# Kernel optimization log

Hardware: AMD Instinct MI355X
Metric: run time of the kernel (lower is better)

## Reference

```python
import jax, jax.numpy as jnp
import numpy as np

N, T, FS, FD, GH, RH, E = 100000, 24, 32, 8, 32, 64, 3200000


def spmm(edge_row, edge_col, edge_val, X):
    # out[i] = sum_e val[e] * X[col[e]]  for edges with row[e]==i
    return jax.ops.segment_sum(edge_val[:, None] * X[edge_col], edge_row, num_segments=N)


def setup_inputs() -> dict:
    key = jax.random.key(0)
    ks = jax.random.split(key, 20)
    s = 0.05
    return {
        "X_static": jax.random.normal(ks[0], (N, FS), jnp.float32),
        "X_dyn_mean": jax.random.normal(ks[1], (T, N, FD), jnp.float32),
        "edge_row": jax.random.randint(ks[2], (E,), 0, N, jnp.int32),
        "edge_col": jax.random.randint(ks[3], (E,), 0, N, jnp.int32),
        "edge_val": jax.random.uniform(ks[4], (E,), jnp.float32),
        # GraphConv layers
        "g1_W": jax.random.normal(ks[5], (GH, FS), jnp.float32) * s,
        "g1_b": jnp.zeros((GH,), jnp.float32),
        "g2_W": jax.random.normal(ks[6], (GH, GH), jnp.float32) * s,
        "g2_b": jnp.zeros((GH,), jnp.float32),
        # GRU (PyTorch layout: 3H rows = [r, z, n])
        "W_ih": jax.random.normal(ks[7], (3 * RH, GH + FD), jnp.float32) * s,
        "W_hh": jax.random.normal(ks[8], (3 * RH, RH), jnp.float32) * s,
        "b_ih": jnp.zeros((3 * RH,), jnp.float32),
        "b_hh": jnp.zeros((3 * RH,), jnp.float32),
        # MLP head
        "h1_W": jax.random.normal(ks[9], (64, RH), jnp.float32) * s,
        "h1_b": jnp.zeros((64,), jnp.float32),
        "h2_W": jax.random.normal(ks[10], (1, 64), jnp.float32) * s,
        "h2_b": jnp.zeros((1,), jnp.float32),
    }


def reference(X_static, X_dyn_mean, edge_row, edge_col, edge_val,
              g1_W, g1_b, g2_W, g2_b, W_ih, W_hh, b_ih, b_hh,
              h1_W, h1_b, h2_W, h2_b):
    # GraphConv x2: linear then sparse A_hat @ Xw, ReLU
    h = jax.nn.relu(spmm(edge_row, edge_col, edge_val, X_static @ g1_W.T + g1_b))
    h = jax.nn.relu(spmm(edge_row, edge_col, edge_val, h @ g2_W.T + g2_b))  # (N, GH)

    # z_t = concat([h, X_dyn_mean[t]], -1); precompute input-gate projections
    z_seq = jnp.concatenate([jnp.broadcast_to(h[None], (T, N, GH)), X_dyn_mean], axis=-1)  # (T,N,GH+FD)
    gi_all = jnp.einsum('tnd,hd->tnh', z_seq, W_ih) + b_ih  # (T,N,3H)

    def step(hs, gi):
        gh = hs @ W_hh.T + b_hh
        i_r, i_z, i_n = jnp.split(gi, 3, axis=-1)
        h_r, h_z, h_n = jnp.split(gh, 3, axis=-1)
        r = jax.nn.sigmoid(i_r + h_r)
        zg = jax.nn.sigmoid(i_z + h_z)
        n = jnp.tanh(i_n + r * h_n)
        h_new = (1.0 - zg) * n + zg * hs
        return h_new, h_new

    h0 = jnp.zeros((N, RH), jnp.float32)
    _, out = jax.lax.scan(step, h0, gi_all)  # (T,N,RH)

    y = jax.nn.relu(out @ h1_W.T + h1_b)
    y = jax.nn.sigmoid(y @ h2_W.T + h2_b)[..., 0]  # (T,N)
    return y
```

## Files before the change

### kernel.cpp

```cpp
#include <hip/hip_runtime.h>
#include <math.h>

typedef short bf16x8_t __attribute__((ext_vector_type(8)));
typedef float f32x4_t  __attribute__((ext_vector_type(4)));

__device__ __forceinline__ float fast_rcp(float x) { return __builtin_amdgcn_rcpf(x); }
__device__ __forceinline__ float sigmoidf_(float x) {
  return fast_rcp(1.0f + __expf(-x));
}
__device__ __forceinline__ float tanhf_(float x) {
  return fmaf(-2.0f, fast_rcp(__expf(2.0f * x) + 1.0f), 1.0f);
}
__device__ __forceinline__ unsigned short f2bf(float f) {
  unsigned int u = __float_as_uint(f);
  unsigned int r = (u + 0x7fffu + ((u >> 16) & 1u)) >> 16;
  return (unsigned short)r;
}
__device__ __forceinline__ float bf2f(unsigned short u) {
  return __uint_as_float(((unsigned int)u) << 16);
}
__device__ __forceinline__ unsigned int cvt_pk_bf16(float a, float b) {
  unsigned int d;
  asm("v_cvt_pk_bf16_f32 %0, %1, %2" : "=v"(d) : "v"(a), "v"(b));
  return d;
}

template<bool RELU_IN, bool OUT_BF16>
__global__ __launch_bounds__(256) void lin32_kernel(
    const float* __restrict__ X, const float* __restrict__ W,
    const float* __restrict__ b, void* __restrict__ outp, int N)
{
  __shared__ float sW[32][33];
  __shared__ float sb[32];
  __shared__ float sX[8][33];
  const int tid = threadIdx.x;
  for (int i = tid; i < 1024; i += 256) sW[i >> 5][i & 31] = W[i];
  if (tid < 32) sb[tid] = b[tid];
  const int n0 = blockIdx.x * 8;
  {
    float v = X[(size_t)n0 * 32 + tid];
    if (RELU_IN) v = fmaxf(v, 0.0f);
    sX[tid >> 5][tid & 31] = v;
  }
  __syncthreads();
  const int ln = tid >> 5, f = tid & 31;
  float acc = sb[f];
  #pragma unroll
  for (int j = 0; j < 32; j++) acc += sX[ln][j] * sW[f][j];
  if (OUT_BF16) ((unsigned short*)outp)[(size_t)n0 * 32 + tid] = f2bf(acc);
  else          ((float*)outp)[(size_t)n0 * 32 + tid] = acc;
}

__global__ __launch_bounds__(256) void spmm_kernel(
    const int* __restrict__ erow, const int* __restrict__ ecol,
    const float* __restrict__ eval, const float* __restrict__ X,
    float* __restrict__ out, int E)
{
  const long gid = (long)blockIdx.x * 256 + threadIdx.x;
  const int e = (int)(gid >> 3);
  const int q = (int)(gid & 7);
  if (e >= E) return;
  const int r = erow[e], c = ecol[e];
  const float v = eval[e];
  const float4 x = *(const float4*)(X + (size_t)c * 32 + q * 4);
  float* o = out + (size_t)r * 32 + q * 4;
  atomicAdd(o + 0, v * x.x);
  atomicAdd(o + 1, v * x.y);
  atomicAdd(o + 2, v * x.z);
  atomicAdd(o + 3, v * x.w);
}

#define BROWS 128
#define BSHIFT 7
#define EPB 8192
#define MAXBUCKETS 1024

__global__ __launch_bounds__(256) void hist_bin_k(
    const int* __restrict__ erow, int* __restrict__ blockHist,
    int E, int nBuckets)
{
  __shared__ int h[MAXBUCKETS];
  for (int i = threadIdx.x; i < nBuckets; i += 256) h[i] = 0;
  __syncthreads();
  const int e0 = blockIdx.x * EPB;
  const int cnt = min(E - e0, EPB);
  for (int i = threadIdx.x; i < cnt; i += 256)
    atomicAdd(&h[erow[e0 + i] >> BSHIFT], 1);
  __syncthreads();
  int* o = blockHist + (size_t)blockIdx.x * nBuckets;
  for (int i = threadIdx.x; i < nBuckets; i += 256) o[i] = h[i];
}

__global__ __launch_bounds__(128) void colscan_k(
    int* __restrict__ blockHist, int* __restrict__ bucketTotal,
    int nb, int nBuckets)
{
  __shared__ int s[128];
  const int b = blockIdx.x;
  const int t = threadIdx.x;
  const int k = (nb + 127) >> 7;
  const int i0 = t * k, i1 = min(nb, i0 + k);
  int p = 0;
  for (int i = i0; i < i1; i++) p += blockHist[(size_t)i * nBuckets + b];
  s[t] = p;
  __syncthreads();
  #pragma unroll
  for (int off = 1; off < 128; off <<= 1) {
    int u = (t >= off) ? s[t - off] : 0;
    __syncthreads(); s[t] += u; __syncthreads();
  }
  int run = s[t] - p;
  if (t == 127) bucketTotal[b] = s[127];
  for (int i = i0; i < i1; i++) {
    int* q = &blockHist[(size_t)i * nBuckets + b];
    int v = *q;
    *q = run;
    run += v;
  }
}

__global__ __launch_bounds__(1024) void bucketstart_k(
    const int* __restrict__ bucketTotal, int* __restrict__ bucketStart,
    int nBuckets)
{
  __shared__ int s[1024];
  const int b = threadIdx.x;
  int v = (b < nBuckets) ? bucketTotal[b] : 0;
  s[b] = v;
  __syncthreads();
  for (int off = 1; off < 1024; off <<= 1) {
    int u = (b >= off) ? s[b - off] : 0;
    __syncthreads(); s[b] += u; __syncthreads();
  }
  if (b < nBuckets) bucketStart[b] = s[b] - v;
  if (b == nBuckets - 1) bucketStart[nBuckets] = s[b];
}

__global__ __launch_bounds__(256) void scatter_stage_k(
    const int* __restrict__ erow, const int* __restrict__ ecol,
    const float* __restrict__ evl, const int* __restrict__ blockOfs,
    const int* __restrict__ bucketStart, int2* __restrict__ binned,
    int E, int nBuckets)
{
  __shared__ int2 rec[EPB];
  __shared__ int  dstv[EPB];
  __shared__ int  cur[MAXBUCKETS];
  __shared__ int  gb[MAXBUCKETS];
  __shared__ int  part[256];
  const int tid = threadIdx.x;
  const int e0 = blockIdx.x * EPB;
  const int cntE = min(E - e0, EPB);
  const int* ofs = blockOfs + (size_t)blockIdx.x * nBuckets;

  for (int i = tid; i < nBuckets; i += 256) cur[i] = 0;
  __syncthreads();
  for (int i = tid; i < cntE; i += 256)
    atomicAdd(&cur[erow[e0 + i] >> BSHIFT], 1);
  __syncthreads();

  const int k = (nBuckets + 255) >> 8;
  const int i0 = tid * k, i1 = min(i0 + k, nBuckets);
  int s = 0;
  for (int i = i0; i < i1; i++) s += cur[i];
  part[tid] = s;
  __syncthreads();
  for (int off = 1; off < 256; off <<= 1) {
    int u = (tid >= off) ? part[tid - off] : 0;
    __syncthreads(); part[tid] += u; __syncthreads();
  }
  int run = part[tid] - s;
  for (int i = i0; i < i1; i++) {
    int hv = cur[i];
    gb[i] = bucketStart[i] + ofs[i] - run;
    cur[i] = run;
    run += hv;
  }
  __syncthreads();

  for (int i = tid; i < cntE; i += 256) {
    int r = erow[e0 + i];
    int c = ecol[e0 + i];
    float v = evl[e0 + i];
    int b = r >> BSHIFT;
    int p = atomicAdd(&cur[b], 1);
    rec[p]  = make_int2(((r & (BROWS - 1)) << 17) | c, __float_as_int(v));
    dstv[p] = gb[b];
  }
  __syncthreads();

  for (int i = tid; i < cntE; i += 256)
    binned[dstv[i] + i] = rec[i];
}

__global__ __launch_bounds__(512) void bucket_sort_k(
    const int* __restrict__ bucketStart, const int2* __restrict__ binned,
    int2* __restrict__ pairs, int* __restrict__ startv, int* __restrict__ cnt,
    int N)
{
  __shared__ int h[BROWS], sc[BROWS], cur[BROWS];
  const int tid = threadIdx.x;
  const int bkt = blockIdx.x;
  const int s = bucketStart[bkt], e = bucketStart[bkt + 1];
  if (tid < BROWS) h[tid] = 0;
  __syncthreads();
  for (int i = s + tid; i < e; i += 512)
    atomicAdd(&h[((unsigned)binned[i].x) >> 17], 1);
  __syncthreads();
  if (tid < BROWS) sc[tid] = h[tid];
  __syncthreads();
  #pragma unroll
  for (int off = 1; off < BROWS; off <<= 1) {
    int u = (tid < BROWS && tid >= off) ? sc[tid - off] : 0;
    __syncthreads();
    if (tid < BROWS) sc[tid] += u;
    __syncthreads();
  }
  if (tid < BROWS) {
    int start = s + sc[tid] - h[tid];
    cur[tid] = start;
    int row = (bkt << BSHIFT) + tid;
    if (row < N) { startv[row] = start; cnt[row] = h[tid]; }
  }
  __syncthreads();
  for (int i = s + tid; i < e; i += 512) {
    int2 r = binned[i];
    int p = atomicAdd(&cur[((unsigned)r.x) >> 17], 1);
    pairs[p] = make_int2(r.x & 0x1ffff, r.y);
  }
}

__global__ __launch_bounds__(256) void hist_k(const int* __restrict__ erow, int* cnt, int E) {
  int e = blockIdx.x * 256 + threadIdx.x;
  if (e < E) atomicAdd(&cnt[erow[e]], 1);
}

__global__ __launch_bounds__(256) void scan1_k(const int* __restrict__ cnt, int* startv, int* bsum, int N) {
  __shared__ int s[256];
  int t = threadIdx.x, i = blockIdx.x * 256 + t;
  int v = (i < N) ? cnt[i] : 0;
  s[t] = v; __syncthreads();
  for (int off = 1; off < 256; off <<= 1) {
    int u = (t >= off) ? s[t - off] : 0;
    __syncthreads(); s[t] += u; __syncthreads();
  }
  if (i < N) startv[i] = s[t] - v;
  if (t == 255) bsum[blockIdx.x] = s[255];
}

__global__ __launch_bounds__(512) void scan2_k(const int* __restrict__ bsum, int* bsumx, int nb) {
  __shared__ int s[512];
  int t = threadIdx.x;
  int v = (t < nb) ? bsum[t] : 0;
  s[t] = v; __syncthreads();
  for (int off = 1; off < 512; off <<= 1) {
    int u = (t >= off) ? s[t - off] : 0;
    __syncthreads(); s[t] += u; __syncthreads();
  }
  if (t < nb) bsumx[t] = s[t] - v;
}

__global__ __launch_bounds__(256) void scan3_k(int* startv, const int* __restrict__ bsumx, int* cursor, int N) {
  int i = blockIdx.x * 256 + threadIdx.x;
  if (i < N) {
    int v = startv[i] + bsumx[i >> 8];
    startv[i] = v;
    cursor[i] = v;
  }
}

__global__ __launch_bounds__(256) void scatter_k(
    const int* __restrict__ erow, const int* __restrict__ ecol,
    const float* __restrict__ evl, int* cursor, int2* __restrict__ pairs, int E)
{
  int e = blockIdx.x * 256 + threadIdx.x;
  if (e < E) {
    int r = erow[e];
    int p = atomicAdd(&cursor[r], 1);
    pairs[p] = make_int2(ecol[e], __float_as_int(evl[e]));
  }
}

__global__ __launch_bounds__(256) void spmm_csr_bf16_k(
    const int* __restrict__ startv, const int* __restrict__ cnt,
    const int2* __restrict__ pairs, const unsigned short* __restrict__ X,
    float* __restrict__ out, int N)
{
  int row = blockIdx.x * 4 + (threadIdx.x >> 6);
  if (row >= N) return;
  int lane = threadIdx.x & 63;
  int f = lane & 31, hh = lane >> 5;
  int start = startv[row];
  int len = cnt[row];
  int half = len >> 1;
  int base = start + (hh ? half : 0);
  int n = hh ? (len - half) : half;
  float acc = 0.0f;
  int i = 0;
  for (; i + 7 < n; i += 8) {
    int2 p0 = pairs[base + i + 0];
    int2 p1 = pairs[base + i + 1];
    int2 p2 = pairs[base + i + 2];
    int2 p3 = pairs[base + i + 3];
    int2 p4 = pairs[base + i + 4];
    int2 p5 = pairs[base + i + 5];
    int2 p6 = pairs[base + i + 6];
    int2 p7 = pairs[base + i + 7];
    float x0 = bf2f(X[(size_t)p0.x * 32 + f]);
    float x1 = bf2f(X[(size_t)p1.x * 32 + f]);
    float x2 = bf2f(X[(size_t)p2.x * 32 + f]);
    float x3 = bf2f(X[(size_t)p3.x * 32 + f]);
    float x4 = bf2f(X[(size_t)p4.x * 32 + f]);
    float x5 = bf2f(X[(size_t)p5.x * 32 + f]);
    float x6 = bf2f(X[(size_t)p6.x * 32 + f]);
    float x7 = bf2f(X[(size_t)p7.x * 32 + f]);
    acc = fmaf(__int_as_float(p0.y), x0, acc);
    acc = fmaf(__int_as_float(p1.y), x1, acc);
    acc = fmaf(__int_as_float(p2.y), x2, acc);
    acc = fmaf(__int_as_float(p3.y), x3, acc);
    acc = fmaf(__int_as_float(p4.y), x4, acc);
    acc = fmaf(__int_as_float(p5.y), x5, acc);
    acc = fmaf(__int_as_float(p6.y), x6, acc);
    acc = fmaf(__int_as_float(p7.y), x7, acc);
  }
  for (; i + 3 < n; i += 4) {
    int2 p0 = pairs[base + i + 0];
    int2 p1 = pairs[base + i + 1];
    int2 p2 = pairs[base + i + 2];
    int2 p3 = pairs[base + i + 3];
    float x0 = bf2f(X[(size_t)p0.x * 32 + f]);
    float x1 = bf2f(X[(size_t)p1.x * 32 + f]);
    float x2 = bf2f(X[(size_t)p2.x * 32 + f]);
    float x3 = bf2f(X[(size_t)p3.x * 32 + f]);
    acc = fmaf(__int_as_float(p0.y), x0, acc);
    acc = fmaf(__int_as_float(p1.y), x1, acc);
    acc = fmaf(__int_as_float(p2.y), x2, acc);
    acc = fmaf(__int_as_float(p3.y), x3, acc);
  }
  for (; i < n; i++) {
    int2 p = pairs[base + i];
    acc = fmaf(__int_as_float(p.y), bf2f(X[(size_t)p.x * 32 + f]), acc);
  }
  acc += __shfl_down(acc, 32);
  if (hh == 0) out[(size_t)row * 32 + f] = acc;
}

#define NB 32

__global__ __launch_bounds__(256, 2) void gru_head_mfma(
    const float* __restrict__ acc2,
    const float* __restrict__ xdyn,
    const float* __restrict__ Wih,
    const float* __restrict__ Whh,
    const float* __restrict__ bih, const float* __restrict__ bhh,
    const float* __restrict__ h1W,
    const float* __restrict__ h1b, const float* __restrict__ h2W,
    const float* __restrict__ h2b,
    float* __restrict__ out, int N, int T)
{
  __shared__ __align__(16) unsigned short z[2][NB][104];
  __shared__ float s_red[2][NB][5];

  const int tid  = threadIdx.x;
  const int w    = tid >> 6;
  const int lane = tid & 63;
  const int ml   = lane & 15;
  const int q    = lane >> 4;
  const int n0   = blockIdx.x * NB;

  bf16x8_t A_r[3], A_z[3], A_in, A_hn[2];
  {
    const int j = 16 * w + ml;
    #pragma unroll
    for (int s = 0; s < 3; s++) {
      union { bf16x8_t v; unsigned short u[8]; } tr, tz;
      #pragma unroll
      for (int jj = 0; jj < 8; jj++) {
        int k = s * 32 + q * 8 + jj;
        float vr = (k < 64) ? Whh[j * 64 + k]        : (k < 72 ? Wih[j * 40 + 32 + (k - 64)] : 0.0f);
        float vz = (k < 64) ? Whh[(64 + j) * 64 + k] : (k < 72 ? Wih[(64 + j) * 40 + 32 + (k - 64)] : 0.0f);
        tr.u[jj] = f2bf(vr);
        tz.u[jj] = f2bf(vz);
      }
      A_r[s] = tr.v; A_z[s] = tz.v;
    }
    union { bf16x8_t v; unsigned short u[8]; } ti;
    #pragma unroll
    for (int jj = 0; jj < 8; jj++) {
      int kk = q * 8 + jj;
      ti.u[jj] = f2bf((kk < 8) ? Wih[(128 + j) * 40 + 32 + kk] : 0.0f);
    }
    A_in = ti.v;
    #pragma unroll
    for (int s = 0; s < 2; s++) {
      union { bf16x8_t v; unsigned short u[8]; } th;
      #pragma unroll
      for (int jj = 0; jj < 8; jj++)
        th.u[jj] = f2bf(Whh[(128 + j) * 64 + s * 32 + q * 8 + jj]);
      A_hn[s] = th.v;
    }
  }
  bf16x8_t Ah[2];
  #pragma unroll
  for (int s = 0; s < 2; s++) {
    union { bf16x8_t v; unsigned short u[8]; } tmp;
    #pragma unroll
    for (int jj = 0; jj < 8; jj++)
      tmp.u[jj] = f2bf(h1W[(16 * w + ml) * 64 + s * 32 + q * 8 + jj]);
    Ah[s] = tmp.v;
  }

  f32x4_t bhhn4, h1b4;
  float h2w_r[4];
  #pragma unroll
  for (int reg = 0; reg < 4; reg++) {
    int j = 16 * w + 4 * q + reg;
    bhhn4[reg] = bhh[128 + j];
    h1b4[reg]  = h1b[j];
    h2w_r[reg] = h2W[j];
  }
  const float h2b0 = h2b[0];

  {
    int nd = tid >> 3, f0 = (tid & 7) * 4;
    float4 v = *(const float4*)(acc2 + (size_t)(n0 + nd) * 32 + f0);
    uint2 pk;
    pk.x = cvt_pk_bf16(fmaxf(v.x, 0.0f), fmaxf(v.y, 0.0f));
    pk.y = cvt_pk_bf16(fmaxf(v.z, 0.0f), fmaxf(v.w, 0.0f));
    *(uint2*)&z[0][nd][f0] = pk;
  }
  __syncthreads();

  f32x4_t gis[3][2];
  {
    bf16x8_t Ag[3];
    #pragma unroll
    for (int g = 0; g < 3; g++) {
      union { bf16x8_t v; unsigned short u[8]; } tmp;
      #pragma unroll
      for (int jj = 0; jj < 8; jj++)
        tmp.u[jj] = f2bf(Wih[(g * 64 + 16 * w + ml) * 40 + q * 8 + jj]);
      Ag[g] = tmp.v;
    }
    bf16x8_t Bg[2];
    #pragma unroll
    for (int nt = 0; nt < 2; nt++)
      Bg[nt] = *(const bf16x8_t*)&z[0][nt * 16 + ml][q * 8];
    f32x4_t zero = {0.0f, 0.0f, 0.0f, 0.0f};
    #pragma unroll
    for (int g = 0; g < 3; g++)
      #pragma unroll
      for (int nt = 0; nt < 2; nt++)
        gis[g][nt] = __builtin_amdgcn_mfma_f32_16x16x32_bf16(Ag[g], Bg[nt], zero, 0, 0, 0);
  }
  __syncthreads();

  for (int i = tid; i < 2 * NB * 104 / 2; i += 256) ((unsigned int*)z)[i] = 0;
  #pragma unroll
  for (int reg = 0; reg < 4; reg++) {
    int j = 16 * w + 4 * q + reg;
    float br = bih[j] + bhh[j];
    float bz = bih[64 + j] + bhh[64 + j];
    float bn = bih[128 + j];
    #pragma unroll
    for (int nt = 0; nt < 2; nt++) {
      gis[0][nt][reg] += br;
      gis[1][nt][reg] += bz;
      gis[2][nt][reg] += bn;
    }
  }
  __syncthreads();

  float hreg[2][4] = {{0, 0, 0, 0}, {0, 0, 0, 0}};

  float4 xv = make_float4(0.f, 0.f, 0.f, 0.f);
  if (tid < 64) xv = *(const float4*)(xdyn + (size_t)n0 * 8 + tid * 4);

  for (int t = 0; t < T; t++) {
    const int b = t & 1;
    if (tid < 64) {
      uint2 pk;
      pk.x = cvt_pk_bf16(xv.x, xv.y);
      pk.y = cvt_pk_bf16(xv.z, xv.w);
      *(uint2*)&z[b][tid >> 1][64 + (tid & 1) * 4] = pk;
      if (t + 1 < T)
        xv = *(const float4*)(xdyn + ((size_t)(t + 1) * N + n0) * 8 + tid * 4);
    }
    __syncthreads();

    if (t >= 2 && tid < 32) {
      float s = s_red[1 - b][tid][0] + s_red[1 - b][tid][1] +
                s_red[1 - b][tid][2] + s_red[1 - b][tid][3];
      out[(size_t)(t - 2) * N + n0 + tid] = sigmoidf_(s + h2b0);
    }

    #pragma unroll
    for (int nt = 0; nt < 2; nt++) {
      bf16x8_t B0 = *(const bf16x8_t*)&z[b][nt * 16 + ml][q * 8];
      bf16x8_t B1 = *(const bf16x8_t*)&z[b][nt * 16 + ml][32 + q * 8];
      bf16x8_t B2 = *(const bf16x8_t*)&z[b][nt * 16 + ml][64 + q * 8];

      f32x4_t ar  = gis[0][nt];
      f32x4_t az  = gis[1][nt];
      f32x4_t ain = gis[2][nt];
      f32x4_t ahn = bhhn4;
      ar  = __builtin_amdgcn_mfma_f32_16x16x32_bf16(A_r[0], B0, ar, 0, 0, 0);
      az  = __builtin_amdgcn_mfma_f32_16x16x32_bf16(A_z[0], B0, az, 0, 0, 0);
      ahn = __builtin_amdgcn_mfma_f32_16x16x32_bf16(A_hn[0], B0, ahn, 0, 0, 0);
      ar  = __builtin_amdgcn_mfma_f32_16x16x32_bf16(A_r[1], B1, ar, 0, 0, 0);
      az  = __builtin_amdgcn_mfma_f32_16x16x32_bf16(A_z[1], B1, az, 0, 0, 0);
      ahn = __builtin_amdgcn_mfma_f32_16x16x32_bf16(A_hn[1], B1, ahn, 0, 0, 0);
      ar  = __builtin_amdgcn_mfma_f32_16x16x32_bf16(A_r[2], B2, ar, 0, 0, 0);
      az  = __builtin_amdgcn_mfma_f32_16x16x32_bf16(A_z[2], B2, az, 0, 0, 0);
      ain = __builtin_amdgcn_mfma_f32_16x16x32_bf16(A_in,  B2, ain, 0, 0, 0);

      if (t >= 1) {
        f32x4_t ha = h1b4;
        ha = __builtin_amdgcn_mfma_f32_16x16x32_bf16(Ah[0], B0, ha, 0, 0, 0);
        ha = __builtin_amdgcn_mfma_f32_16x16x32_bf16(Ah[1], B1, ha, 0, 0, 0);
        float p = 0.0f;
        #pragma unroll
        for (int reg = 0; reg < 4; reg++)
          p += h2w_r[reg] * fmaxf(ha[reg], 0.0f);
        p += __shfl_xor(p, 16, 64);
        p += __shfl_xor(p, 32, 64);
        if (q == 0) s_red[b][nt * 16 + ml][w] = p;
      }

      float hv[4];
      #pragma unroll
      for (int reg = 0; reg < 4; reg++) {
        float r  = sigmoidf_(ar[reg]);
        float zg = sigmoidf_(az[reg]);
        float nn = tanhf_(fmaf(r, ahn[reg], ain[reg]));
        float h  = fmaf(zg, hreg[nt][reg] - nn, nn);
        hreg[nt][reg] = h;
        hv[reg] = h;
      }
      uint2 pk;
      pk.x = cvt_pk_bf16(hv[0], hv[1]);
      pk.y = cvt_pk_bf16(hv[2], hv[3]);
      *(uint2*)&z[1 - b][nt * 16 + ml][16 * w + 4 * q] = pk;
    }
  }

  const int bl = (T - 1) & 1;
  __syncthreads();

  if (tid < 32) {
    float s = s_red[bl][tid][0] + s_red[bl][tid][1] +
              s_red[bl][tid][2] + s_red[bl][tid][3];
    out[(size_t)(T - 2) * N + n0 + tid] = sigmoidf_(s + h2b0);
  }
  #pragma unroll
  for (int nt = 0; nt < 2; nt++) {
    bf16x8_t B0 = *(const bf16x8_t*)&z[1 - bl][nt * 16 + ml][q * 8];
    bf16x8_t B1 = *(const bf16x8_t*)&z[1 - bl][nt * 16 + ml][32 + q * 8];
    f32x4_t ha = h1b4;
    ha = __builtin_amdgcn_mfma_f32_16x16x32_bf16(Ah[0], B0, ha, 0, 0, 0);
    ha = __builtin_amdgcn_mfma_f32_16x16x32_bf16(Ah[1], B1, ha, 0, 0, 0);
    float p = 0.0f;
    #pragma unroll
    for (int reg = 0; reg < 4; reg++)
      p += h2w_r[reg] * fmaxf(ha[reg], 0.0f);
    p += __shfl_xor(p, 16, 64);
    p += __shfl_xor(p, 32, 64);
    if (q == 0) s_red[1 - bl][nt * 16 + ml][w] = p;
  }
  __syncthreads();
  if (tid < 32) {
    float s = s_red[1 - bl][tid][0] + s_red[1 - bl][tid][1] +
              s_red[1 - bl][tid][2] + s_red[1 - bl][tid][3];
    out[(size_t)(T - 1) * N + n0 + tid] = sigmoidf_(s + h2b0);
  }
}

extern "C" void kernel_launch(void* const* d_in, const int* in_sizes, int n_in,
                              void* d_out, int out_size, void* d_ws, size_t ws_size,
                              hipStream_t stream) {
  const float* Xs   = (const float*)d_in[0];
  const float* Xd   = (const float*)d_in[1];
  const int*   erow = (const int*)d_in[2];
  const int*   ecol = (const int*)d_in[3];
  const float* evl  = (const float*)d_in[4];
  const float* g1W  = (const float*)d_in[5];
  const float* g1b  = (const float*)d_in[6];
  const float* g2W  = (const float*)d_in[7];
  const float* g2b  = (const float*)d_in[8];
  const float* Wih  = (const float*)d_in[9];
  const float* Whh  = (const float*)d_in[10];
  const float* bih  = (const float*)d_in[11];
  const float* bhh  = (const float*)d_in[12];
  const float* h1W  = (const float*)d_in[13];
  const float* h1b  = (const float*)d_in[14];
  const float* h2W  = (const float*)d_in[15];
  const float* h2b  = (const float*)d_in[16];

  const int N = in_sizes[0] / 32;
  const int E = in_sizes[2];
  const int T = in_sizes[1] / (N * 8);

  float* out  = (float*)d_out;
  char*  base = (char*)d_ws;
  float* buf0 = (float*)base;
  float* buf1 = buf0 + (size_t)N * 32;
  int*   cnt    = (int*)(buf1 + (size_t)N * 32);
  int*   startv = cnt + N;
  int*   cursor = startv + N;
  int*   bsum   = cursor + N;
  int*   bsumx  = bsum + 512;
  unsigned short* buf0h = (unsigned short*)buf0;

  const int nBuckets = (N + BROWS - 1) >> BSHIFT;
  const int nbBin    = (E + EPB - 1) / EPB;

  int* bucketStart = bsumx + 512;
  int* bucketTotal = bucketStart + nBuckets + 1;
  int* blockHist   = bucketTotal + nBuckets;
  char* pp = (char*)(blockHist + (size_t)nbBin * nBuckets);
  pp = (char*)(((uintptr_t)pp + 15) & ~(uintptr_t)15);
  int2* pairs  = (int2*)pp;
  int2* binned = pairs + E;

  const size_t neededA = (size_t)((char*)(binned + E) - base);
  const size_t neededB = (size_t)((char*)(pairs + E) - base);

  const int linBlocks = (N + 7) / 8;
  const int eBlocks   = (E + 255) / 256;
  const int nb1       = (N + 255) / 256;

  const bool tierA = (ws_size >= neededA) && (nBuckets <= MAXBUCKETS) &&
                     (N <= (1 << 17));
  const bool tierB = !tierA && (ws_size >= neededB);

  if (tierA) {
    lin32_kernel<false, true><<<linBlocks, 256, 0, stream>>>(Xs, g1W, g1b, buf0h, N);

    hist_bin_k<<<nbBin, 256, 0, stream>>>(erow, blockHist, E, nBuckets);
    colscan_k<<<nBuckets, 128, 0, stream>>>(blockHist, bucketTotal, nbBin, nBuckets);
    bucketstart_k<<<1, 1024, 0, stream>>>(bucketTotal, bucketStart, nBuckets);
    scatter_stage_k<<<nbBin, 256, 0, stream>>>(erow, ecol, evl, blockHist,
                                               bucketStart, binned, E, nBuckets);
    bucket_sort_k<<<nBuckets, 512, 0, stream>>>(bucketStart, binned, pairs,
                                                startv, cnt, N);

    spmm_csr_bf16_k<<<(N + 3) / 4, 256, 0, stream>>>(startv, cnt, pairs, buf0h, buf1, N);
    lin32_kernel<true, true><<<linBlocks, 256, 0, stream>>>(buf1, g2W, g2b, buf0h, N);
    spmm_csr_bf16_k<<<(N + 3) / 4, 256, 0, stream>>>(startv, cnt, pairs, buf0h, buf1, N);
  } else if (tierB) {
    lin32_kernel<false, true><<<linBlocks, 256, 0, stream>>>(Xs, g1W, g1b, buf0h, N);

    hipMemsetAsync(cnt, 0, (size_t)N * sizeof(int), stream);
    hist_k<<<eBlocks, 256, 0, stream>>>(erow, cnt, E);
    scan1_k<<<nb1, 256, 0, stream>>>(cnt, startv, bsum, N);
    scan2_k<<<1, 512, 0, stream>>>(bsum, bsumx, nb1);
    scan3_k<<<nb1, 256, 0, stream>>>(startv, bsumx, cursor, N);
    scatter_k<<<eBlocks, 256, 0, stream>>>(erow, ecol, evl, cursor, pairs, E);

    spmm_csr_bf16_k<<<(N + 3) / 4, 256, 0, stream>>>(startv, cnt, pairs, buf0h, buf1, N);
    lin32_kernel<true, true><<<linBlocks, 256, 0, stream>>>(buf1, g2W, g2b, buf0h, N);
    spmm_csr_bf16_k<<<(N + 3) / 4, 256, 0, stream>>>(startv, cnt, pairs, buf0h, buf1, N);
  } else {
    lin32_kernel<false, false><<<linBlocks, 256, 0, stream>>>(Xs, g1W, g1b, buf0, N);
    const int spmmBlocks = (int)(((long)E * 8 + 255) / 256);
    hipMemsetAsync(buf1, 0, (size_t)N * 32 * sizeof(float), stream);
    spmm_kernel<<<spmmBlocks, 256, 0, stream>>>(erow, ecol, evl, buf0, buf1, E);
    lin32_kernel<true, false><<<linBlocks, 256, 0, stream>>>(buf1, g2W, g2b, buf0, N);
    hipMemsetAsync(buf1, 0, (size_t)N * 32 * sizeof(float), stream);
    spmm_kernel<<<spmmBlocks, 256, 0, stream>>>(erow, ecol, evl, buf0, buf1, E);
  }

  gru_head_mfma<<<N / NB, 256, 0, stream>>>(buf1, Xd, Wih, Whh, bih, bhh,
                                            h1W, h1b, h2W, h2b, out, N, T);
}
```

Baseline: 596.4 us.

## Fuse linear layers into hist and SpMM kernels, prescale GRU weights for exp2

Merges the first linear projection into the histogram kernel launch and fuses the second ReLU+linear into the first SpMM's epilogue, dropping two kernel launches and an intermediate fp32 round trip. The GRU weights and biases are prescaled by -log2e or 2*log2e so the sigmoid and tanh use raw exp2 with no multiply. Buffers are swapped so the final SpMM writes to buf0. The scaled weights are rounded to bf16 after scaling, which slightly changes numerics, and the fused SpMM adds shared-memory weight loads to every block.

```diff
diff --git a/kernel.cpp b/kernel.cpp
--- a/kernel.cpp
+++ b/kernel.cpp
@@ -3,13 +3,18 @@
 
 typedef short bf16x8_t __attribute__((ext_vector_type(8)));
 typedef float f32x4_t  __attribute__((ext_vector_type(4)));
+
+#define LOG2E 1.4426950408889634f
 
 __device__ __forceinline__ float fast_rcp(float x) { return __builtin_amdgcn_rcpf(x); }
 __device__ __forceinline__ float sigmoidf_(float x) {
   return fast_rcp(1.0f + __expf(-x));
 }
-__device__ __forceinline__ float tanhf_(float x) {
-  return fmaf(-2.0f, fast_rcp(__expf(2.0f * x) + 1.0f), 1.0f);
+__device__ __forceinline__ float sigmoid2n_(float y) {
+  return fast_rcp(1.0f + __builtin_amdgcn_exp2f(y));
+}
+__device__ __forceinline__ float tanh2n_(float y) {
+  return fmaf(-2.0f, fast_rcp(__builtin_amdgcn_exp2f(y) + 1.0f), 1.0f);
 }
 __device__ __forceinline__ unsigned short f2bf(float f) {
   unsigned int u = __float_as_uint(f);
@@ -75,20 +80,41 @@
 #define EPB 8192
 #define MAXBUCKETS 1024
 
-__global__ __launch_bounds__(256) void hist_bin_k(
+__global__ __launch_bounds__(256) void lin_hist_k(
+    const float* __restrict__ X, const float* __restrict__ W,
+    const float* __restrict__ b, unsigned short* __restrict__ outp,
+    int N, int linBlocks,
     const int* __restrict__ erow, int* __restrict__ blockHist,
     int E, int nBuckets)
 {
+  __shared__ float sW[32][33];
+  __shared__ float sb[32];
+  __shared__ float sX[8][33];
   __shared__ int h[MAXBUCKETS];
-  for (int i = threadIdx.x; i < nBuckets; i += 256) h[i] = 0;
-  __syncthreads();
-  const int e0 = blockIdx.x * EPB;
-  const int cnt = min(E - e0, EPB);
-  for (int i = threadIdx.x; i < cnt; i += 256)
-    atomicAdd(&h[erow[e0 + i] >> BSHIFT], 1);
-  __syncthreads();
-  int* o = blockHist + (size_t)blockIdx.x * nBuckets;
-  for (int i = threadIdx.x; i < nBuckets; i += 256) o[i] = h[i];
+  const int tid = threadIdx.x;
+  if ((int)blockIdx.x < linBlocks) {
+    for (int i = tid; i < 1024; i += 256) sW[i >> 5][i & 31] = W[i];
+    if (tid < 32) sb[tid] = b[tid];
+    const int n0 = blockIdx.x * 8;
+    sX[tid >> 5][tid & 31] = X[(size_t)n0 * 32 + tid];
+    __syncthreads();
+    const int ln = tid >> 5, f = tid & 31;
+    float acc = sb[f];
+    #pragma unroll
+    for (int j = 0; j < 32; j++) acc += sX[ln][j] * sW[f][j];
+    outp[(size_t)n0 * 32 + tid] = f2bf(acc);
+  } else {
+    const int bid = blockIdx.x - linBlocks;
+    for (int i = tid; i < nBuckets; i += 256) h[i] = 0;
+    __syncthreads();
+    const int e0 = bid * EPB;
+    const int cnt = min(E - e0, EPB);
+    for (int i = tid; i < cnt; i += 256)
+      atomicAdd(&h[erow[e0 + i] >> BSHIFT], 1);
+    __syncthreads();
+    int* o = blockHist + (size_t)bid * nBuckets;
+    for (int i = tid; i < nBuckets; i += 256) o[i] = h[i];
+  }
 }
 
 __global__ __launch_bounds__(128) void colscan_k(
@@ -280,14 +306,25 @@
   }
 }
 
+template<bool FUSE_LIN>
 __global__ __launch_bounds__(256) void spmm_csr_bf16_k(
     const int* __restrict__ startv, const int* __restrict__ cnt,
     const int2* __restrict__ pairs, const unsigned short* __restrict__ X,
-    float* __restrict__ out, int N)
-{
-  int row = blockIdx.x * 4 + (threadIdx.x >> 6);
+    void* __restrict__ outp, const float* __restrict__ W,
+    const float* __restrict__ b, int N)
+{
+  __shared__ float sW[32][33];
+  __shared__ float sb[32];
+  __shared__ float sAcc[4][32];
+  const int tid = threadIdx.x;
+  if (FUSE_LIN) {
+    for (int i = tid; i < 1024; i += 256) sW[i >> 5][i & 31] = W[i];
+    if (tid < 32) sb[tid] = b[tid];
+    __syncthreads();
+  }
+  int row = blockIdx.x * 4 + (tid >> 6);
   if (row >= N) return;
-  int lane = threadIdx.x & 63;
+  int lane = tid & 63;
   int f = lane & 31, hh = lane >> 5;
   int start = startv[row];
   int len = cnt[row];
@@ -341,7 +378,21 @@
     acc = fmaf(__int_as_float(p.y), bf2f(X[(size_t)p.x * 32 + f]), acc);
   }
   acc += __shfl_down(acc, 32);
-  if (hh == 0) out[(size_t)row * 32 + f] = acc;
+  if (!FUSE_LIN) {
+    if (hh == 0) ((float*)outp)[(size_t)row * 32 + f] = acc;
+  } else {
+    const int w = tid >> 6;
+    if (hh == 0) sAcc[w][f] = fmaxf(acc, 0.0f);
+    float part = 0.0f;
+    #pragma unroll
+    for (int j0 = 0; j0 < 16; j0++) {
+      int j = hh * 16 + j0;
+      part = fmaf(sAcc[w][j], sW[f][j], part);
+    }
+    part += __shfl_down(part, 32);
+    if (hh == 0)
+      ((unsigned short*)outp)[(size_t)row * 32 + f] = f2bf(sb[f] + part);
+  }
 }
 
 #define NB 32
@@ -367,6 +418,9 @@
   const int q    = lane >> 4;
   const int n0   = blockIdx.x * NB;
 
+  const float SR = -LOG2E;
+  const float SN = 2.0f * LOG2E;
+
   bf16x8_t A_r[3], A_z[3], A_in, A_hn[2];
   {
     const int j = 16 * w + ml;
@@ -378,8 +432,8 @@
         int k = s * 32 + q * 8 + jj;
         float vr = (k < 64) ? Whh[j * 64 + k]        : (k < 72 ? Wih[j * 40 + 32 + (k - 64)] : 0.0f);
         float vz = (k < 64) ? Whh[(64 + j) * 64 + k] : (k < 72 ? Wih[(64 + j) * 40 + 32 + (k - 64)] : 0.0f);
-        tr.u[jj] = f2bf(vr);
-        tz.u[jj] = f2bf(vz);
+        tr.u[jj] = f2bf(SR * vr);
+        tz.u[jj] = f2bf(SR * vz);
       }
       A_r[s] = tr.v; A_z[s] = tz.v;
     }
@@ -387,7 +441,7 @@
     #pragma unroll
     for (int jj = 0; jj < 8; jj++) {
       int kk = q * 8 + jj;
-      ti.u[jj] = f2bf((kk < 8) ? Wih[(128 + j) * 40 + 32 + kk] : 0.0f);
+      ti.u[jj] = f2bf((kk < 8) ? SN * Wih[(128 + j) * 40 + 32 + kk] : 0.0f);
     }
     A_in = ti.v;
     #pragma unroll
@@ -395,7 +449,7 @@
       union { bf16x8_t v; unsigned short u[8]; } th;
       #pragma unroll
       for (int jj = 0; jj < 8; jj++)
-        th.u[jj] = f2bf(Whh[(128 + j) * 64 + s * 32 + q * 8 + jj]);
+        th.u[jj] = f2bf(SN * Whh[(128 + j) * 64 + s * 32 + q * 8 + jj]);
       A_hn[s] = th.v;
     }
   }
@@ -414,11 +468,11 @@
   #pragma unroll
   for (int reg = 0; reg < 4; reg++) {
     int j = 16 * w + 4 * q + reg;
-    bhhn4[reg] = bhh[128 + j];
+    bhhn4[reg] = SN * bhh[128 + j];
     h1b4[reg]  = h1b[j];
-    h2w_r[reg] = h2W[j];
-  }
-  const float h2b0 = h2b[0];
+    h2w_r[reg] = SR * h2W[j];
+  }
+  const float h2b0 = SR * h2b[0];
 
   {
     int nd = tid >> 3, f0 = (tid & 7) * 4;
@@ -435,10 +489,11 @@
     bf16x8_t Ag[3];
     #pragma unroll
     for (int g = 0; g < 3; g++) {
+      const float sg = (g < 2) ? SR : SN;
       union { bf16x8_t v; unsigned short u[8]; } tmp;
       #pragma unroll
       for (int jj = 0; jj < 8; jj++)
-        tmp.u[jj] = f2bf(Wih[(g * 64 + 16 * w + ml) * 40 + q * 8 + jj]);
+        tmp.u[jj] = f2bf(sg * Wih[(g * 64 + 16 * w + ml) * 40 + q * 8 + jj]);
       Ag[g] = tmp.v;
     }
     bf16x8_t Bg[2];
@@ -458,9 +513,9 @@
   #pragma unroll
   for (int reg = 0; reg < 4; reg++) {
     int j = 16 * w + 4 * q + reg;
-    float br = bih[j] + bhh[j];
-    float bz = bih[64 + j] + bhh[64 + j];
-    float bn = bih[128 + j];
+    float br = SR * (bih[j] + bhh[j]);
+    float bz = SR * (bih[64 + j] + bhh[64 + j]);
+    float bn = SN * bih[128 + j];
     #pragma unroll
     for (int nt = 0; nt < 2; nt++) {
       gis[0][nt][reg] += br;
@@ -490,7 +545,7 @@
     if (t >= 2 && tid < 32) {
       float s = s_red[1 - b][tid][0] + s_red[1 - b][tid][1] +
                 s_red[1 - b][tid][2] + s_red[1 - b][tid][3];
-      out[(size_t)(t - 2) * N + n0 + tid] = sigmoidf_(s + h2b0);
+      out[(size_t)(t - 2) * N + n0 + tid] = sigmoid2n_(s + h2b0);
     }
 
     #pragma unroll
@@ -529,9 +584,9 @@
       float hv[4];
       #pragma unroll
       for (int reg = 0; reg < 4; reg++) {
-        float r  = sigmoidf_(ar[reg]);
-        float zg = sigmoidf_(az[reg]);
-        float nn = tanhf_(fmaf(r, ahn[reg], ain[reg]));
+        float r  = sigmoid2n_(ar[reg]);
+        float zg = sigmoid2n_(az[reg]);
+        float nn = tanh2n_(fmaf(r, ahn[reg], ain[reg]));
         float h  = fmaf(zg, hreg[nt][reg] - nn, nn);
         hreg[nt][reg] = h;
         hv[reg] = h;
@@ -549,7 +604,7 @@
   if (tid < 32) {
     float s = s_red[bl][tid][0] + s_red[bl][tid][1] +
               s_red[bl][tid][2] + s_red[bl][tid][3];
-    out[(size_t)(T - 2) * N + n0 + tid] = sigmoidf_(s + h2b0);
+    out[(size_t)(T - 2) * N + n0 + tid] = sigmoid2n_(s + h2b0);
   }
   #pragma unroll
   for (int nt = 0; nt < 2; nt++) {
@@ -570,7 +625,7 @@
   if (tid < 32) {
     float s = s_red[1 - bl][tid][0] + s_red[1 - bl][tid][1] +
               s_red[1 - bl][tid][2] + s_red[1 - bl][tid][3];
-    out[(size_t)(T - 1) * N + n0 + tid] = sigmoidf_(s + h2b0);
+    out[(size_t)(T - 1) * N + n0 + tid] = sigmoid2n_(s + h2b0);
   }
 }
 
@@ -609,6 +664,7 @@
   int*   bsum   = cursor + N;
   int*   bsumx  = bsum + 512;
   unsigned short* buf0h = (unsigned short*)buf0;
+  unsigned short* buf1h = (unsigned short*)buf1;
 
   const int nBuckets = (N + BROWS - 1) >> BSHIFT;
   const int nbBin    = (E + EPB - 1) / EPB;
@@ -633,9 +689,9 @@
   const bool tierB = !tierA && (ws_size >= neededB);
 
   if (tierA) {
-    lin32_kernel<false, true><<<linBlocks, 256, 0, stream>>>(Xs, g1W, g1b, buf0h, N);
-
-    hist_bin_k<<<nbBin, 256, 0, stream>>>(erow, blockHist, E, nBuckets);
+    lin_hist_k<<<linBlocks + nbBin, 256, 0, stream>>>(
+        Xs, g1W, g1b, buf0h, N, linBlocks, erow, blockHist, E, nBuckets);
+
     colscan_k<<<nBuckets, 128, 0, stream>>>(blockHist, bucketTotal, nbBin, nBuckets);
     bucketstart_k<<<1, 1024, 0, stream>>>(bucketTotal, bucketStart, nBuckets);
     scatter_stage_k<<<nbBin, 256, 0, stream>>>(erow, ecol, evl, blockHist,
@@ -643,9 +699,10 @@
     bucket_sort_k<<<nBuckets, 512, 0, stream>>>(bucketStart, binned, pairs,
                                                 startv, cnt, N);
 
-    spmm_csr_bf16_k<<<(N + 3) / 4, 256, 0, stream>>>(startv, cnt, pairs, buf0h, buf1, N);
-    lin32_kernel<true, true><<<linBlocks, 256, 0, stream>>>(buf1, g2W, g2b, buf0h, N);
-    spmm_csr_bf16_k<<<(N + 3) / 4, 256, 0, stream>>>(startv, cnt, pairs, buf0h, buf1, N);
+    spmm_csr_bf16_k<true><<<(N + 3) / 4, 256, 0, stream>>>(
+        startv, cnt, pairs, buf0h, buf1h, g2W, g2b, N);
+    spmm_csr_bf16_k<false><<<(N + 3) / 4, 256, 0, stream>>>(
+        startv, cnt, pairs, buf1h, buf0, nullptr, nullptr, N);
   } else if (tierB) {
     lin32_kernel<false, true><<<linBlocks, 256, 0, stream>>>(Xs, g1W, g1b, buf0h, N);
 
@@ -656,19 +713,20 @@
     scan3_k<<<nb1, 256, 0, stream>>>(startv, bsumx, cursor, N);
     scatter_k<<<eBlocks, 256, 0, stream>>>(erow, ecol, evl, cursor, pairs, E);
 
-    spmm_csr_bf16_k<<<(N + 3) / 4, 256, 0, stream>>>(startv, cnt, pairs, buf0h, buf1, N);
-    lin32_kernel<true, true><<<linBlocks, 256, 0, stream>>>(buf1, g2W, g2b, buf0h, N);
-    spmm_csr_bf16_k<<<(N + 3) / 4, 256, 0, stream>>>(startv, cnt, pairs, buf0h, buf1, N);
+    spmm_csr_bf16_k<true><<<(N + 3) / 4, 256, 0, stream>>>(
+        startv, cnt, pairs, buf0h, buf1h, g2W, g2b, N);
+    spmm_csr_bf16_k<false><<<(N + 3) / 4, 256, 0, stream>>>(
+        startv, cnt, pairs, buf1h, buf0, nullptr, nullptr, N);
   } else {
-    lin32_kernel<false, false><<<linBlocks, 256, 0, stream>>>(Xs, g1W, g1b, buf0, N);
+    lin32_kernel<false, false><<<linBlocks, 256, 0, stream>>>(Xs, g1W, g1b, buf1, N);
     const int spmmBlocks = (int)(((long)E * 8 + 255) / 256);
-    hipMemsetAsync(buf1, 0, (size_t)N * 32 * sizeof(float), stream);
-    spmm_kernel<<<spmmBlocks, 256, 0, stream>>>(erow, ecol, evl, buf0, buf1, E);
-    lin32_kernel<true, false><<<linBlocks, 256, 0, stream>>>(buf1, g2W, g2b, buf0, N);
-    hipMemsetAsync(buf1, 0, (size_t)N * 32 * sizeof(float), stream);
-    spmm_kernel<<<spmmBlocks, 256, 0, stream>>>(erow, ecol, evl, buf0, buf1, E);
-  }
-
-  gru_head_mfma<<<N / NB, 256, 0, stream>>>(buf1, Xd, Wih, Whh, bih, bhh,
+    hipMemsetAsync(buf0, 0, (size_t)N * 32 * sizeof(float), stream);
+    spmm_kernel<<<spmmBlocks, 256, 0, stream>>>(erow, ecol, evl, buf1, buf0, E);
+    lin32_kernel<true, false><<<linBlocks, 256, 0, stream>>>(buf0, g2W, g2b, buf1, N);
+    hipMemsetAsync(buf0, 0, (size_t)N * 32 * sizeof(float), stream);
+    spmm_kernel<<<spmmBlocks, 256, 0, stream>>>(erow, ecol, evl, buf1, buf0, E);
+  }
+
+  gru_head_mfma<<<N / NB, 256, 0, stream>>>(buf0, Xd, Wih, Whh, bih, bhh,
                                             h1W, h1b, h2W, h2b, out, N, T);
 }
```

New measurement: 625.1 us. 4.8% more time.
